# Kernel tuning notes

Hardware: AMD Instinct MI355X
Metric: run time of the kernel (lower is better)

## Reference

```python
import jax, jax.numpy as jnp
import numpy as np

N, K, FEAT = 64, 32, 1024      # nodes, neighbors per node, input feature dim
C1, F1 = 4, 16                 # layer1: out_channels=4, out_features=hidden[0]/4=16
C2, F2 = 32, 1                 # layer2: out_channels=hidden[1]=32, out_features=1
NUM_CLASS = 10
BN_EPS = 1e-5


def _sgnroot(x):
    return jnp.sign(x) * jnp.sqrt(jnp.clip(jnp.abs(x), 1e-8))


def _feature_adjacency(x, nb):
    # x: (N,c,f), nb: (N,K,c,f) -> adj: (N,c,f,f)
    fadj = jnp.einsum('nca,nkcb->ncab', x, nb)          # sum over K neighbors
    fadj = fadj + jnp.swapaxes(fadj, -2, -1)
    s = _sgnroot(fadj)
    out = s / (jnp.abs(s).sum(axis=1, keepdims=True) + 1e-7)  # row-normalize over channel dim
    return jnp.where(jnp.isnan(out), 0.0, out)


def _layer(x, nb, W, c_out, f_out):
    # FeatTrans1d.forward: adjacency build + batched matmul + full-width conv (== dense contraction)
    n = x.shape[0]
    adj = _feature_adjacency(x, nb)                     # (N,c,f,f)
    xa = jnp.einsum('ncab,ncb->nca', adj, x)            # adj @ x
    x2 = jnp.einsum('ocf,ncf->no', W, xa).reshape(n, c_out, f_out)
    na = jnp.einsum('ncab,nkcb->nkca', adj, nb)         # per-node adj applied to its neighbors
    nb2 = jnp.einsum('ocf,nkcf->nko', W, na).reshape(n, -1, c_out, f_out)
    return x2, nb2


def _bn_softsign_x(x, w, b):
    # BatchNorm1d (training stats over batch+feature dims) + Softsign; x: (N,C,F)
    m = x.mean(axis=(0, 2), keepdims=True)
    v = x.var(axis=(0, 2), keepdims=True)
    y = (x - m) / jnp.sqrt(v + BN_EPS) * w[None, :, None] + b[None, :, None]
    return y / (1.0 + jnp.abs(y))


def _bn_softsign_nb(x, w, b):
    # each node's neighbor set is normalized independently (list comprehension in original); x: (N,K,C,F)
    m = x.mean(axis=(1, 3), keepdims=True)
    v = x.var(axis=(1, 3), keepdims=True)
    y = (x - m) / jnp.sqrt(v + BN_EPS) * w[None, None, :, None] + b[None, None, :, None]
    return y / (1.0 + jnp.abs(y))


def setup_inputs() -> dict:
    key = jax.random.key(0)
    ks = jax.random.split(key, 6)
    return {
        'x': jax.random.normal(ks[0], (N, 1, FEAT), jnp.float32),
        'neighbor': jax.random.normal(ks[1], (N, K, 1, FEAT), jnp.float32),
        'W1': jax.random.normal(ks[2], (C1 * F1, 1, FEAT), jnp.float32) * (1.0 / FEAT) ** 0.5,
        'W2': jax.random.normal(ks[3], (C2 * F2, C1, F1), jnp.float32) * (1.0 / (C1 * F1)) ** 0.5,
        'bn1_w': jnp.ones((C1,), jnp.float32),
        'bn1_b': jnp.zeros((C1,), jnp.float32),
        'bn2_w': jnp.ones((C2,), jnp.float32),
        'bn2_b': jnp.zeros((C2,), jnp.float32),
        'lin_w': jax.random.normal(ks[4], (NUM_CLASS, C2 * F2), jnp.float32) * (1.0 / (C2 * F2)) ** 0.5,
        'lin_b': jnp.zeros((NUM_CLASS,), jnp.float32),
    }


def reference(x, neighbor, W1, W2, bn1_w, bn1_b, bn2_w, bn2_b, lin_w, lin_b):
    x1, nb1 = _layer(x, neighbor, W1, C1, F1)           # (N,4,16), (N,K,4,16)
    x1 = _bn_softsign_x(x1, bn1_w, bn1_b)
    nb1 = _bn_softsign_nb(nb1, bn1_w, bn1_b)
    x2, _ = _layer(x1, nb1, W2, C2, F2)                 # (N,32,1)
    x2 = _bn_softsign_x(x2, bn2_w, bn2_b)
    return x2.reshape(x2.shape[0], -1) @ lin_w.T + lin_b  # (N,NUM_CLASS)
```

## Files before the change

### kernel.cpp

```cpp
#include <hip/hip_runtime.h>

typedef unsigned short u16;
typedef short short8 __attribute__((ext_vector_type(8)));
typedef float floatx4 __attribute__((ext_vector_type(4)));
typedef float floatx2 __attribute__((ext_vector_type(2)));
typedef unsigned int uintx4 __attribute__((ext_vector_type(4)));
typedef unsigned int uintx2 __attribute__((ext_vector_type(2)));
typedef u16 ushortx4 __attribute__((ext_vector_type(4)));

#define FEAT 1024
#define KNB  32

__device__ __forceinline__ u16 f2bf(float f) {
    unsigned u = __float_as_uint(f);
    u += 0x7fffu + ((u >> 16) & 1u);
    return (u16)(u >> 16);
}
__device__ __forceinline__ unsigned pack2bf(float a, float b) {
    return (unsigned)f2bf(a) | ((unsigned)f2bf(b) << 16);
}
__device__ __forceinline__ float softsign(float v) { return v / (1.f + fabsf(v)); }

union Frag { uintx4 q; unsigned d[4]; short8 v; };

__global__ __launch_bounds__(256, 2) void k2_main(
    const float* __restrict__ xg, const float* __restrict__ nbg,
    const float* __restrict__ w1g, float* __restrict__ pws)
{
    __shared__ float sS[FEAT];
    __shared__ float sX[FEAT];
    __shared__ u16  sY[34 * 1024];

    const int t = threadIdx.x;
    const int bid = blockIdx.x;
    const int n = bid & 63;
    const int chunk = bid >> 6;
    const int chunkbase = chunk * 128;
    const int w = t >> 6;
    const int l = t & 63;
    const int m = l & 15;
    const int g = l >> 4;

    {
        ushortx4 z4 = {0, 0, 0, 0};
        *(ushortx4*)&sY[33 * 1024 + t * 4] = z4;
    }
    {
        floatx4 xv = *(const floatx4*)(xg + (size_t)n * FEAT + t * 4);
        *(floatx4*)&sX[t * 4] = xv;
        ushortx4 xb4 = {f2bf(xv[0]), f2bf(xv[1]), f2bf(xv[2]), f2bf(xv[3])};
        *(ushortx4*)&sY[t * 4] = xb4;
    }
    {
        const float* nbase = nbg + ((size_t)n * KNB) * FEAT + t * 4;
        floatx4 sacc = {0.f, 0.f, 0.f, 0.f};
        #pragma unroll 4
        for (int k = 0; k < KNB; ++k) {
            floatx4 v = *(const floatx4*)(nbase + (size_t)k * FEAT);
            sacc += v;
            int row = k + 1;
            int c16 = (t >> 1) ^ (row & 7);
            ushortx4 p4 = {f2bf(v[0]), f2bf(v[1]), f2bf(v[2]), f2bf(v[3])};
            *(ushortx4*)&sY[row * 1024 + c16 * 8 + (t & 1) * 4] = p4;
        }
        *(floatx4*)&sS[t * 4] = sacc;
    }

    const float xa0 = xg[(size_t)n * FEAT + chunkbase + w * 32 + m];
    const float xa1 = xg[(size_t)n * FEAT + chunkbase + w * 32 + 16 + m];
    __syncthreads();
    const float Sa0 = sS[chunkbase + w * 32 + m];
    const float Sa1 = sS[chunkbase + w * 32 + 16 + m];

    const u16* b2base = (m == 0) ? &sY[32 * 1024] : &sY[33 * 1024];
    const int sw = (m & 7);

    floatx4 acc[2][3];
    #pragma unroll
    for (int i = 0; i < 2; ++i)
        #pragma unroll
        for (int j = 0; j < 3; ++j) { floatx4 z = {0.f, 0.f, 0.f, 0.f}; acc[i][j] = z; }

    const floatx2 vxa0 = {xa0, xa0}, vxa1 = {xa1, xa1};
    const floatx2 vSa0 = {Sa0, Sa0}, vSa1 = {Sa1, Sa1};

    #pragma unroll 2
    for (int s = 0; s < 32; ++s) {
        const int bloc = s * 32 + g * 8;
        const int cidx = bloc >> 3;

        floatx4 xq0 = *(const floatx4*)&sX[bloc];
        floatx4 xq1 = *(const floatx4*)&sX[bloc + 4];
        floatx4 sq0 = *(const floatx4*)&sS[bloc];
        floatx4 sq1 = *(const floatx4*)&sS[bloc + 4];

        Frag af0, af1;
        #pragma unroll
        for (int p = 0; p < 4; ++p) {
            floatx2 xbp = (p < 2) ? ((p == 0) ? (floatx2){xq0[0], xq0[1]} : (floatx2){xq0[2], xq0[3]})
                                  : ((p == 2) ? (floatx2){xq1[0], xq1[1]} : (floatx2){xq1[2], xq1[3]});
            floatx2 sbp = (p < 2) ? ((p == 0) ? (floatx2){sq0[0], sq0[1]} : (floatx2){sq0[2], sq0[3]})
                                  : ((p == 2) ? (floatx2){sq1[0], sq1[1]} : (floatx2){sq1[2], sq1[3]});
            floatx2 u0 = xbp * vSa0 + sbp * vxa0;
            floatx2 u1 = xbp * vSa1 + sbp * vxa1;
            uintx2 b0b = __builtin_bit_cast(uintx2, u0);
            uintx2 b1b = __builtin_bit_cast(uintx2, u1);
            af0.d[p] = 0x3F803F80u | (b0b.y & 0x80000000u) | ((b0b.x >> 16) & 0x8000u);
            af1.d[p] = 0x3F803F80u | (b1b.y & 0x80000000u) | ((b1b.x >> 16) & 0x8000u);
        }

        Frag b0, b1, b2;
        b0.q = *(const uintx4*)&sY[ m       * 1024 + ((cidx ^ sw) << 3)];
        b1.q = *(const uintx4*)&sY[(16 + m) * 1024 + ((cidx ^ sw) << 3)];
        b2.q = *(const uintx4*)&b2base[cidx << 3];

        acc[0][0] = __builtin_amdgcn_mfma_f32_16x16x32_bf16(af0.v, b0.v, acc[0][0], 0, 0, 0);
        acc[0][1] = __builtin_amdgcn_mfma_f32_16x16x32_bf16(af0.v, b1.v, acc[0][1], 0, 0, 0);
        acc[0][2] = __builtin_amdgcn_mfma_f32_16x16x32_bf16(af0.v, b2.v, acc[0][2], 0, 0, 0);
        acc[1][0] = __builtin_amdgcn_mfma_f32_16x16x32_bf16(af1.v, b0.v, acc[1][0], 0, 0, 0);
        acc[1][1] = __builtin_amdgcn_mfma_f32_16x16x32_bf16(af1.v, b1.v, acc[1][1], 0, 0, 0);
        acc[1][2] = __builtin_amdgcn_mfma_f32_16x16x32_bf16(af1.v, b2.v, acc[1][2], 0, 0, 0);
    }
    __syncthreads();

    u16* sZ = sY;
    #pragma unroll
    for (int ti = 0; ti < 2; ++ti)
        #pragma unroll
        for (int jt = 0; jt < 3; ++jt) {
            int j = jt * 16 + m;
            int aloc = w * 32 + ti * 16 + g * 4;
            ushortx4 zz;
            zz.x = f2bf(acc[ti][jt][0]);
            zz.y = f2bf(acc[ti][jt][1]);
            zz.z = f2bf(acc[ti][jt][2]);
            zz.w = f2bf(acc[ti][jt][3]);
            *(ushortx4*)&sZ[j * 136 + aloc] = zz;
        }
    __syncthreads();

    floatx4 a2[3];
    #pragma unroll
    for (int j = 0; j < 3; ++j) { floatx4 z = {0.f, 0.f, 0.f, 0.f}; a2[j] = z; }
    #pragma unroll
    for (int kc = 0; kc < 4; ++kc) {
        const float* wsrc = w1g + (size_t)(w * 16 + m) * FEAT + chunkbase + kc * 32 + g * 8;
        floatx4 wf0 = *(const floatx4*)wsrc;
        floatx4 wf1 = *(const floatx4*)(wsrc + 4);
        Frag wb;
        wb.d[0] = pack2bf(wf0[0], wf0[1]);
        wb.d[1] = pack2bf(wf0[2], wf0[3]);
        wb.d[2] = pack2bf(wf1[0], wf1[1]);
        wb.d[3] = pack2bf(wf1[2], wf1[3]);
        #pragma unroll
        for (int jt = 0; jt < 3; ++jt) {
            Frag za;
            za.q = *(const uintx4*)&sZ[(jt * 16 + m) * 136 + kc * 32 + g * 8];
            a2[jt] = __builtin_amdgcn_mfma_f32_16x16x32_bf16(za.v, wb.v, a2[jt], 0, 0, 0);
        }
    }
    float* pbase = pws + (size_t)(n * 8 + chunk) * 33 * 64;
    #pragma unroll
    for (int jt = 0; jt < 3; ++jt)
        #pragma unroll
        for (int r = 0; r < 4; ++r) {
            int j = jt * 16 + g * 4 + r;
            if (j < 33) pbase[j * 64 + w * 16 + m] = a2[jt][r];
        }
}

__global__ __launch_bounds__(256, 1) void kB(
    const float* __restrict__ pws, const float* __restrict__ bn1w,
    const float* __restrict__ bn1b, const float* __restrict__ w2g,
    float* __restrict__ x22ws)
{
    __shared__ float sx2[64 * 64];
    __shared__ float snb[32 * 64];
    __shared__ float sx1[64], sS1[64], sadj[4 * 16 * 16], sxa[64];
    __shared__ float ssc[4], sbi[4], ssc2[4], sbi2[4];
    const int t = threadIdx.x;
    const int n = blockIdx.x;

    #pragma unroll
    for (int r = 0; r < 4; ++r) {
        int slot = t + r * 256;
        int nn = slot >> 4, oc = slot & 15;
        const float* p = pws + (size_t)nn * 16896 + oc * 4;
        floatx4 tmp[8];
        #pragma unroll
        for (int c = 0; c < 8; ++c) tmp[c] = *(const floatx4*)(p + c * 2112);
        floatx4 s01 = tmp[0] + tmp[1], s23 = tmp[2] + tmp[3];
        floatx4 s45 = tmp[4] + tmp[5], s67 = tmp[6] + tmp[7];
        *(floatx4*)&sx2[slot * 4] = (s01 + s23) + (s45 + s67);
    }
    #pragma unroll
    for (int r = 0; r < 2; ++r) {
        int slot = t + r * 256;
        int k = slot >> 4, oc = slot & 15;
        const float* p = pws + (size_t)n * 16896 + (1 + k) * 64 + oc * 4;
        floatx4 tmp[8];
        #pragma unroll
        for (int c = 0; c < 8; ++c) tmp[c] = *(const floatx4*)(p + c * 2112);
        floatx4 s01 = tmp[0] + tmp[1], s23 = tmp[2] + tmp[3];
        floatx4 s45 = tmp[4] + tmp[5], s67 = tmp[6] + tmp[7];
        *(floatx4*)&snb[slot * 4] = (s01 + s23) + (s45 + s67);
    }
    __syncthreads();
    {
        int cc = t >> 6, l2 = t & 63;
        float s = 0.f, s2 = 0.f;
        #pragma unroll
        for (int i = 0; i < 16; ++i) {
            int idx = l2 * 16 + i;
            int nn = idx >> 4, f = idx & 15;
            float v = sx2[nn * 64 + cc * 16 + f];
            s += v; s2 += v * v;
        }
        float s3 = 0.f, s4 = 0.f;
        #pragma unroll
        for (int i = 0; i < 8; ++i) {
            int idx = l2 * 8 + i;
            int k = idx >> 4, f = idx & 15;
            float v = snb[k * 64 + cc * 16 + f];
            s3 += v; s4 += v * v;
        }
        #pragma unroll
        for (int off = 32; off > 0; off >>= 1) {
            s  += __shfl_down(s, off);  s2 += __shfl_down(s2, off);
            s3 += __shfl_down(s3, off); s4 += __shfl_down(s4, off);
        }
        if (l2 == 0) {
            float wv = bn1w[cc], bv = bn1b[cc];
            float mean = s * (1.f / 1024.f);
            float var = s2 * (1.f / 1024.f) - mean * mean;
            float rs = rsqrtf(var + 1e-5f);
            ssc[cc] = rs * wv;
            sbi[cc] = bv - mean * rs * wv;
            float mean2 = s3 * (1.f / 512.f);
            float var2 = s4 * (1.f / 512.f) - mean2 * mean2;
            float rs2 = rsqrtf(var2 + 1e-5f);
            ssc2[cc] = rs2 * wv;
            sbi2[cc] = bv - mean2 * rs2 * wv;
        }
    }
    __syncthreads();
    if (t < 64) {
        int cc = t >> 4;
        sx1[t] = softsign(sx2[n * 64 + t] * ssc[cc] + sbi[cc]);
        float a = 0.f;
        for (int k = 0; k < KNB; ++k)
            a += softsign(snb[k * 64 + t] * ssc2[cc] + sbi2[cc]);
        sS1[t] = a;
    }
    __syncthreads();
    {
        int a = t >> 4, b = t & 15;
        float sc[4]; float den = 1e-7f;
        #pragma unroll
        for (int c = 0; c < 4; ++c) {
            float u = sx1[c * 16 + a] * sS1[c * 16 + b] + sx1[c * 16 + b] * sS1[c * 16 + a];
            float r = sqrtf(fmaxf(fabsf(u), 1e-8f));
            sc[c] = copysignf(r, u);
            den += r;
        }
        float inv = 1.f / den;
        #pragma unroll
        for (int c = 0; c < 4; ++c) sadj[(c * 16 + a) * 16 + b] = sc[c] * inv;
    }
    __syncthreads();
    if (t < 64) {
        int cc = t >> 4;
        float a = 0.f;
        #pragma unroll
        for (int b = 0; b < 16; ++b) a += sadj[t * 16 + b] * sx1[cc * 16 + b];
        sxa[t] = a;
    }
    __syncthreads();
    if (t < 32) {
        float a = 0.f;
        #pragma unroll
        for (int cf = 0; cf < 64; ++cf) a += w2g[t * 64 + cf] * sxa[cf];
        x22ws[n * 32 + t] = a;
    }
}

__global__ __launch_bounds__(256) void kC(
    const float* __restrict__ x22ws, const float* __restrict__ bn2w,
    const float* __restrict__ bn2b, const float* __restrict__ linw,
    const float* __restrict__ linb, float* __restrict__ outg)
{
    __shared__ float sy[64 * 32];
    __shared__ float ssc[32], sbi[32];
    __shared__ float sx[64 * 32];
    const int t = threadIdx.x;
    #pragma unroll
    for (int r = 0; r < 8; ++r) sx[t + r * 256] = x22ws[t + r * 256];
    __syncthreads();
    if (t < 32) {
        float s = 0.f, s2 = 0.f;
        for (int nn = 0; nn < 64; ++nn) {
            float v = sx[nn * 32 + t];
            s += v; s2 += v * v;
        }
        float mean = s * (1.f / 64.f);
        float var = s2 * (1.f / 64.f) - mean * mean;
        float rs = rsqrtf(var + 1e-5f);
        float wv = bn2w[t], bv = bn2b[t];
        ssc[t] = rs * wv;
        sbi[t] = bv - mean * rs * wv;
    }
    __syncthreads();
    #pragma unroll
    for (int r = 0; r < 8; ++r) {
        int idx = t + r * 256;
        int o = idx & 31;
        sy[idx] = softsign(sx[idx] * ssc[o] + sbi[o]);
    }
    __syncthreads();
    for (int r = 0; r < 3; ++r) {
        int idx = t + r * 256;
        if (idx < 640) {
            int nn = idx / 10, cls = idx % 10;
            float a = linb[cls];
            #pragma unroll
            for (int o = 0; o < 32; ++o) a += sy[nn * 32 + o] * linw[cls * 32 + o];
            outg[idx] = a;
        }
    }
}

extern "C" void kernel_launch(void* const* d_in, const int* in_sizes, int n_in,
                              void* d_out, int out_size, void* d_ws, size_t ws_size,
                              hipStream_t stream) {
    (void)in_sizes; (void)n_in; (void)out_size; (void)ws_size;
    const float* xg   = (const float*)d_in[0];
    const float* nbg  = (const float*)d_in[1];
    const float* w1g  = (const float*)d_in[2];
    const float* w2g  = (const float*)d_in[3];
    const float* bn1w = (const float*)d_in[4];
    const float* bn1b = (const float*)d_in[5];
    const float* bn2w = (const float*)d_in[6];
    const float* bn2b = (const float*)d_in[7];
    const float* linw = (const float*)d_in[8];
    const float* linb = (const float*)d_in[9];

    float* pws   = (float*)d_ws;
    float* x22ws = pws + (size_t)64 * 8 * 33 * 64;
    float* outg  = (float*)d_out;

    k2_main<<<dim3(512), dim3(256), 0, stream>>>(xg, nbg, w1g, pws);
    kB<<<dim3(64), dim3(256), 0, stream>>>(pws, bn1w, bn1b, w2g, x22ws);
    kC<<<dim3(1), dim3(256), 0, stream>>>(x22ws, bn2w, bn2b, linw, linb, outg);
}
```

Before: 103.5 us.

## Pre-convert neighbor tiles to bf16 in a separate kernel and DMA them into LDS

Adds a k1_conv pre-pass that converts each node's neighbor and x rows to swizzled bf16 once and writes partial neighbor sums to workspace. k2_main then fills its LDS tile with global_load_lds direct copies and sums 8 partials, instead of each of the 8 chunk blocks per node re-reading and converting 128KB of fp32 neighbors. This cuts the redundant global traffic and conversion work in k2_main, at the cost of an extra kernel launch and a round trip through workspace memory.

```diff
diff --git a/kernel.cpp b/kernel.cpp
--- a/kernel.cpp
+++ b/kernel.cpp
@@ -21,11 +21,68 @@
 }
 __device__ __forceinline__ float softsign(float v) { return v / (1.f + fabsf(v)); }
 
+__device__ __forceinline__ void gload_lds16(const void* g, void* l) {
+    __builtin_amdgcn_global_load_lds(
+        (const __attribute__((address_space(1))) unsigned int*)g,
+        (__attribute__((address_space(3))) unsigned int*)l, 16, 0, 0);
+}
+
 union Frag { uintx4 q; unsigned d[4]; short8 v; };
 
+__global__ __launch_bounds__(256) void k1_conv(
+    const float* __restrict__ xg, const float* __restrict__ nbg,
+    u16* __restrict__ ybf, float* __restrict__ spart)
+{
+    const int t = threadIdx.x;
+    const int bid = blockIdx.x;
+    const int n = bid & 63;
+    const int rc = bid >> 6;
+    u16* yb = ybf + (size_t)n * 34816;
+    const int r0 = rc * 4 + 1;
+
+    #pragma unroll
+    for (int p = 0; p < 2; ++p) {
+        int row = r0 + p * 2 + (t >> 7);
+        int cc = t & 127;
+        const float* src = nbg + (size_t)(n * KNB + row - 1) * FEAT + cc * 8;
+        floatx4 v0 = *(const floatx4*)src;
+        floatx4 v1 = *(const floatx4*)(src + 4);
+        uintx4 pk;
+        pk.x = pack2bf(v0[0], v0[1]);
+        pk.y = pack2bf(v0[2], v0[3]);
+        pk.z = pack2bf(v1[0], v1[1]);
+        pk.w = pack2bf(v1[2], v1[3]);
+        *(uintx4*)&yb[row * 1024 + ((cc ^ (row & 7)) << 3)] = pk;
+    }
+    {
+        const float* sb = nbg + (size_t)(n * KNB + r0 - 1) * FEAT + t * 4;
+        floatx4 a  = *(const floatx4*)sb;
+        floatx4 b  = *(const floatx4*)(sb + FEAT);
+        floatx4 c2 = *(const floatx4*)(sb + 2 * FEAT);
+        floatx4 d  = *(const floatx4*)(sb + 3 * FEAT);
+        *(floatx4*)&spart[(size_t)(n * 8 + rc) * 1024 + t * 4] = (a + b) + (c2 + d);
+    }
+    if (rc == 0 && t < 128) {
+        const float* src = xg + (size_t)n * FEAT + t * 8;
+        floatx4 v0 = *(const floatx4*)src;
+        floatx4 v1 = *(const floatx4*)(src + 4);
+        uintx4 pk;
+        pk.x = pack2bf(v0[0], v0[1]);
+        pk.y = pack2bf(v0[2], v0[3]);
+        pk.z = pack2bf(v1[0], v1[1]);
+        pk.w = pack2bf(v1[2], v1[3]);
+        *(uintx4*)&yb[t << 3] = pk;
+    }
+    if (rc == 7 && t < 128) {
+        uintx4 z = {0, 0, 0, 0};
+        *(uintx4*)&yb[33 * 1024 + (t << 3)] = z;
+    }
+}
+
 __global__ __launch_bounds__(256, 2) void k2_main(
-    const float* __restrict__ xg, const float* __restrict__ nbg,
-    const float* __restrict__ w1g, float* __restrict__ pws)
+    const float* __restrict__ xg, const float* __restrict__ w1g,
+    const u16* __restrict__ ybf, const float* __restrict__ spart,
+    float* __restrict__ pws)
 {
     __shared__ float sS[FEAT];
     __shared__ float sX[FEAT];
@@ -42,28 +99,19 @@
     const int g = l >> 4;
 
     {
-        ushortx4 z4 = {0, 0, 0, 0};
-        *(ushortx4*)&sY[33 * 1024 + t * 4] = z4;
-    }
-    {
-        floatx4 xv = *(const floatx4*)(xg + (size_t)n * FEAT + t * 4);
-        *(floatx4*)&sX[t * 4] = xv;
-        ushortx4 xb4 = {f2bf(xv[0]), f2bf(xv[1]), f2bf(xv[2]), f2bf(xv[3])};
-        *(ushortx4*)&sY[t * 4] = xb4;
-    }
-    {
-        const float* nbase = nbg + ((size_t)n * KNB) * FEAT + t * 4;
-        floatx4 sacc = {0.f, 0.f, 0.f, 0.f};
-        #pragma unroll 4
-        for (int k = 0; k < KNB; ++k) {
-            floatx4 v = *(const floatx4*)(nbase + (size_t)k * FEAT);
-            sacc += v;
-            int row = k + 1;
-            int c16 = (t >> 1) ^ (row & 7);
-            ushortx4 p4 = {f2bf(v[0]), f2bf(v[1]), f2bf(v[2]), f2bf(v[3])};
-            *(ushortx4*)&sY[row * 1024 + c16 * 8 + (t & 1) * 4] = p4;
-        }
-        *(floatx4*)&sS[t * 4] = sacc;
+        const char* ysrc = (const char*)(ybf + (size_t)n * 34816);
+        char* ydst = (char*)sY;
+        #pragma unroll
+        for (int j2 = 0; j2 < 17; ++j2)
+            gload_lds16(ysrc + j2 * 4096 + w * 1024 + l * 16,
+                        ydst + j2 * 4096 + w * 1024);
+        gload_lds16((const char*)(xg + (size_t)n * FEAT) + w * 1024 + l * 16,
+                    (char*)sX + w * 1024);
+        const float* sp = spart + (size_t)n * 8192 + t * 4;
+        floatx4 a = {0.f, 0.f, 0.f, 0.f};
+        #pragma unroll
+        for (int c2 = 0; c2 < 8; ++c2) a += *(const floatx4*)(sp + c2 * 1024);
+        *(floatx4*)&sS[t * 4] = a;
     }
 
     const float xa0 = xg[(size_t)n * FEAT + chunkbase + w * 32 + m];
@@ -346,9 +394,12 @@
 
     float* pws   = (float*)d_ws;
     float* x22ws = pws + (size_t)64 * 8 * 33 * 64;
+    u16*   ybf   = (u16*)((char*)d_ws + 4333568);
+    float* spart = (float*)((char*)d_ws + 8790016);
     float* outg  = (float*)d_out;
 
-    k2_main<<<dim3(512), dim3(256), 0, stream>>>(xg, nbg, w1g, pws);
+    k1_conv<<<dim3(512), dim3(256), 0, stream>>>(xg, nbg, ybf, spart);
+    k2_main<<<dim3(512), dim3(256), 0, stream>>>(xg, w1g, ybf, spart, pws);
     kB<<<dim3(64), dim3(256), 0, stream>>>(pws, bn1w, bn1b, w2g, x22ws);
     kC<<<dim3(1), dim3(256), 0, stream>>>(x22ws, bn2w, bn2b, linw, linb, outg);
 }
```

Result: slower. 106.1 us (+2.6%).

## Fuse final BN/linear kernel into kB via last-block counter; prefetch W1

Applied to the files above, without the earlier changes.

Merges the single-block kC kernel into kB using an atomic counter, so the last block to finish performs the second BatchNorm, softsign and linear layer. This removes one kernel launch. The counter is reset inside k2_main. W1 fragments are now loaded at the start of k2_main to hide their latency, and the neighbor loop unroll goes from 4 to 8. The relaxed-ordering counter with a manual waitcnt adds a memory-ordering risk, and the prefetch raises register pressure.

```diff
diff --git a/kernel.cpp b/kernel.cpp
--- a/kernel.cpp
+++ b/kernel.cpp
@@ -25,7 +25,8 @@
 
 __global__ __launch_bounds__(256, 2) void k2_main(
     const float* __restrict__ xg, const float* __restrict__ nbg,
-    const float* __restrict__ w1g, float* __restrict__ pws)
+    const float* __restrict__ w1g, float* __restrict__ pws,
+    unsigned int* __restrict__ cnt)
 {
     __shared__ float sS[FEAT];
     __shared__ float sX[FEAT];
@@ -41,6 +42,19 @@
     const int m = l & 15;
     const int g = l >> 4;
 
+    if (bid == 0 && t == 0)
+        __hip_atomic_store(cnt, 0u, __ATOMIC_RELAXED, __HIP_MEMORY_SCOPE_AGENT);
+
+    floatx4 wpre[8];
+    {
+        const float* wbase = w1g + (size_t)(w * 16 + m) * FEAT + chunkbase + g * 8;
+        #pragma unroll
+        for (int kc = 0; kc < 4; ++kc) {
+            wpre[kc * 2]     = *(const floatx4*)(wbase + kc * 32);
+            wpre[kc * 2 + 1] = *(const floatx4*)(wbase + kc * 32 + 4);
+        }
+    }
+
     {
         ushortx4 z4 = {0, 0, 0, 0};
         *(ushortx4*)&sY[33 * 1024 + t * 4] = z4;
@@ -54,7 +68,7 @@
     {
         const float* nbase = nbg + ((size_t)n * KNB) * FEAT + t * 4;
         floatx4 sacc = {0.f, 0.f, 0.f, 0.f};
-        #pragma unroll 4
+        #pragma unroll 8
         for (int k = 0; k < KNB; ++k) {
             floatx4 v = *(const floatx4*)(nbase + (size_t)k * FEAT);
             sacc += v;
@@ -144,9 +158,8 @@
     for (int j = 0; j < 3; ++j) { floatx4 z = {0.f, 0.f, 0.f, 0.f}; a2[j] = z; }
     #pragma unroll
     for (int kc = 0; kc < 4; ++kc) {
-        const float* wsrc = w1g + (size_t)(w * 16 + m) * FEAT + chunkbase + kc * 32 + g * 8;
-        floatx4 wf0 = *(const floatx4*)wsrc;
-        floatx4 wf1 = *(const floatx4*)(wsrc + 4);
+        floatx4 wf0 = wpre[kc * 2];
+        floatx4 wf1 = wpre[kc * 2 + 1];
         Frag wb;
         wb.d[0] = pack2bf(wf0[0], wf0[1]);
         wb.d[1] = pack2bf(wf0[2], wf0[3]);
@@ -169,15 +182,19 @@
         }
 }
 
-__global__ __launch_bounds__(256, 1) void kB(
+__global__ __launch_bounds__(256, 1) void kBC(
     const float* __restrict__ pws, const float* __restrict__ bn1w,
     const float* __restrict__ bn1b, const float* __restrict__ w2g,
-    float* __restrict__ x22ws)
+    const float* __restrict__ bn2w, const float* __restrict__ bn2b,
+    const float* __restrict__ linw, const float* __restrict__ linb,
+    float* __restrict__ x22ws, unsigned int* __restrict__ cnt,
+    float* __restrict__ outg)
 {
     __shared__ float sx2[64 * 64];
     __shared__ float snb[32 * 64];
     __shared__ float sx1[64], sS1[64], sadj[4 * 16 * 16], sxa[64];
     __shared__ float ssc[4], sbi[4], ssc2[4], sbi2[4];
+    __shared__ int lastflag;
     const int t = threadIdx.x;
     const int n = blockIdx.x;
 
@@ -280,41 +297,45 @@
         float a = 0.f;
         #pragma unroll
         for (int cf = 0; cf < 64; ++cf) a += w2g[t * 64 + cf] * sxa[cf];
-        x22ws[n * 32 + t] = a;
-    }
-}
-
-__global__ __launch_bounds__(256) void kC(
-    const float* __restrict__ x22ws, const float* __restrict__ bn2w,
-    const float* __restrict__ bn2b, const float* __restrict__ linw,
-    const float* __restrict__ linb, float* __restrict__ outg)
-{
-    __shared__ float sy[64 * 32];
-    __shared__ float ssc[32], sbi[32];
-    __shared__ float sx[64 * 32];
-    const int t = threadIdx.x;
-    #pragma unroll
-    for (int r = 0; r < 8; ++r) sx[t + r * 256] = x22ws[t + r * 256];
+        __hip_atomic_store(&x22ws[n * 32 + t], a,
+                           __ATOMIC_RELAXED, __HIP_MEMORY_SCOPE_AGENT);
+    }
+
+    asm volatile("s_waitcnt vmcnt(0)" ::: "memory");
+    __syncthreads();
+    if (t == 0)
+        lastflag = (int)__hip_atomic_fetch_add(cnt, 1u,
+                        __ATOMIC_RELAXED, __HIP_MEMORY_SCOPE_AGENT);
+    __syncthreads();
+    if (lastflag != 63) return;
+
+    float* const sy   = snb;
+    float* const sx3  = sx2;
+    float* const ssc3 = sx1;
+    float* const sbi3 = sS1;
+
+    #pragma unroll
+    for (int r = 0; r < 8; ++r) sx3[t + r * 256] = x22ws[t + r * 256];
     __syncthreads();
     if (t < 32) {
         float s = 0.f, s2 = 0.f;
         for (int nn = 0; nn < 64; ++nn) {
-            float v = sx[nn * 32 + t];
+            float v = sx3[nn * 32 + t];
             s += v; s2 += v * v;
         }
         float mean = s * (1.f / 64.f);
         float var = s2 * (1.f / 64.f) - mean * mean;
         float rs = rsqrtf(var + 1e-5f);
         float wv = bn2w[t], bv = bn2b[t];
-        ssc[t] = rs * wv;
-        sbi[t] = bv - mean * rs * wv;
+        ssc3[t] = rs * wv;
+        sbi3[t] = bv - mean * rs * wv;
     }
     __syncthreads();
     #pragma unroll
     for (int r = 0; r < 8; ++r) {
         int idx = t + r * 256;
         int o = idx & 31;
-        sy[idx] = softsign(sx[idx] * ssc[o] + sbi[o]);
+        sy[idx] = softsign(sx3[idx] * ssc3[o] + sbi3[o]);
     }
     __syncthreads();
     for (int r = 0; r < 3; ++r) {
@@ -346,9 +367,10 @@
 
     float* pws   = (float*)d_ws;
     float* x22ws = pws + (size_t)64 * 8 * 33 * 64;
+    unsigned int* cnt = (unsigned int*)(x22ws + 64 * 32);
     float* outg  = (float*)d_out;
 
-    k2_main<<<dim3(512), dim3(256), 0, stream>>>(xg, nbg, w1g, pws);
-    kB<<<dim3(64), dim3(256), 0, stream>>>(pws, bn1w, bn1b, w2g, x22ws);
-    kC<<<dim3(1), dim3(256), 0, stream>>>(x22ws, bn2w, bn2b, linw, linb, outg);
-}
+    k2_main<<<dim3(512), dim3(256), 0, stream>>>(xg, nbg, w1g, pws, cnt);
+    kBC<<<dim3(64), dim3(256), 0, stream>>>(pws, bn1w, bn1b, w2g, bn2w, bn2b,
+                                            linw, linb, x22ws, cnt, outg);
+}
```

Result: no change. 104.1 us (+0.6%).
